# Kernel tuning notes

Hardware: AMD Instinct MI355X
Metric: run time of the kernel (lower is better)

## Reference

```python
import jax, jax.numpy as jnp
import numpy as np

B, H, W = 16, 128, 128
NUM_SAMPLES, HID = 16, 256


def setup_inputs() -> dict:
    key = jax.random.key(0)
    ks = jax.random.split(key, 12)
    inp = {
        "x": jax.random.uniform(ks[0], (B, H, W, 2), jnp.float32) * 2.0 - 1.0,
        "sample_idx": jax.random.randint(ks[1], (B,), 0, NUM_SAMPLES),
        "shift_vectors": jax.random.normal(ks[2], (NUM_SAMPLES, 2), jnp.float32) * 0.05,
        "rotation_angle": jax.random.normal(ks[3], (NUM_SAMPLES, 1), jnp.float32) * 0.05,
        "color_scales": 1.0 + jax.random.normal(ks[4], (NUM_SAMPLES, 3), jnp.float32) * 0.05,
        "color_shifts": jax.random.normal(ks[5], (NUM_SAMPLES, 3), jnp.float32) * 0.05,
        "W1": jax.random.normal(ks[6], (2, HID), jnp.float32) / np.sqrt(2.0),
        "b1": jnp.zeros((HID,), jnp.float32),
        "W2": jax.random.normal(ks[7], (HID, HID), jnp.float32) / np.sqrt(HID),
        "b2": jnp.zeros((HID,), jnp.float32),
        "W3": jax.random.normal(ks[8], (HID, HID), jnp.float32) / np.sqrt(HID),
        "b3": jnp.zeros((HID,), jnp.float32),
        "W4": jax.random.normal(ks[9], (HID, 3), jnp.float32) / np.sqrt(HID),
        "b4": jnp.zeros((3,), jnp.float32),
    }
    return inp


def reference(x, sample_idx, shift_vectors, rotation_angle, color_scales, color_shifts,
              W1, b1, W2, b2, W3, b3, W4, b4):
    # Per-sample affine coordinate transform (vectorized gather + batched 2x3 affine).
    shift = shift_vectors[sample_idx]            # [B,2] -> (dy, dx)
    dy, dx = shift[:, 0], shift[:, 1]
    ang = rotation_angle[sample_idx, 0]          # [B]
    c, s = jnp.cos(ang), jnp.sin(ang)
    rot = jnp.stack([jnp.stack([c, -s], -1),
                     jnp.stack([s, c], -1)], -2)  # [B,2,2]
    trans = jnp.stack([dx, dy], -1)               # [B,2]
    coords = jnp.einsum('bij,bhwj->bhwi', rot, x) + trans[:, None, None, :]

    # INR decoder MLP: coords -> RGB
    h = jax.nn.relu(coords @ W1 + b1)
    h = jax.nn.relu(h @ W2 + b2)
    h = jax.nn.relu(h @ W3 + b3)
    out = h @ W4 + b4                             # [B,H,W,3]

    # Per-sample color affine, skipped for reference sample idx==0.
    scales = color_scales[sample_idx][:, None, None, :]
    shifts = color_shifts[sample_idx][:, None, None, :]
    mask = (sample_idx != 0)[:, None, None, None]
    out = jnp.where(mask, out * scales + shifts, out)
    return out, dx, dy
```

## Files before the change

### kernel.cpp

```cpp
#include <hip/hip_runtime.h>
#include <math.h>

typedef _Float16 half8  __attribute__((ext_vector_type(8)));
typedef _Float16 half4v __attribute__((ext_vector_type(4)));
typedef __fp16   fp16x2 __attribute__((ext_vector_type(2)));
typedef float    f32x4  __attribute__((ext_vector_type(4)));
typedef float    f32x16 __attribute__((ext_vector_type(16)));

#define W1OFF 0
#define W2OFF 4096
#define W3OFF 69632
#define W4OFF 135168
#define SWTOT 143360
#define OUT_PIX (16*128*128)

__global__ void inr_prep(const float* __restrict__ W1, const float* __restrict__ W2,
                         const float* __restrict__ W3, const float* __restrict__ W4,
                         const int* __restrict__ sidx, const float* __restrict__ sv,
                         _Float16* __restrict__ wsw, float* __restrict__ outtail)
{
    int tid = blockIdx.x * 256 + threadIdx.x;
    if (tid < 16) {
        int si = sidx[tid];
        outtail[tid]      = sv[2*si + 1];
        outtail[16 + tid] = sv[2*si + 0];
    }
    if (tid >= SWTOT) return;
    int kind, rel;
    if      (tid < W2OFF) { kind = 0; rel = tid; }
    else if (tid < W3OFF) { kind = 1; rel = tid - W2OFF; }
    else if (tid < W4OFF) { kind = 2; rel = tid - W3OFF; }
    else                  { kind = 3; rel = tid - W4OFF; }
    int j    = rel & 7;
    int lane = (rel >> 3) & 63;
    int blk  = rel >> 9;
    int m32  = lane & 31;
    int hsel = lane >> 5;
    float val;
    if (kind == 3) {
        int k = blk*16 + hsel*8 + j;
        val = (m32 < 3) ? W4[k*3 + m32] : 0.0f;
    } else if (kind == 0) {
        int m = blk*32 + m32;
        int k = hsel*8 + j;
        val = (k < 2) ? W1[k*256 + m] : 0.0f;
    } else {
        int MT = blk & 7, s = blk >> 3;
        int m = MT*32 + m32;
        int k = s*16 + hsel*8 + j;
        val = (kind == 1) ? W2[k*256 + m] : W3[k*256 + m];
    }
    wsw[tid] = (_Float16)val;
}

template<int NKS>
__device__ __forceinline__ void do_layer(const half8* __restrict__ Asw,
                                         const float* __restrict__ bias,
                                         _Float16* hbuf, int w, int m32, int hsel, int lane)
{
    f32x16 acc[2][4];
#pragma unroll
    for (int mt = 0; mt < 2; ++mt)
#pragma unroll
        for (int nt = 0; nt < 4; ++nt)
#pragma unroll
            for (int i = 0; i < 16; ++i)
                acc[mt][nt][i] = 0.0f;

#pragma unroll
    for (int s = 0; s < NKS; ++s) {
        half8 aw[2];
#pragma unroll
        for (int mt = 0; mt < 2; ++mt)
            aw[mt] = Asw[(s*8 + 2*w + mt)*64 + lane];
        half8 bf[4];
        int g = s*2 + hsel;
#pragma unroll
        for (int nt = 0; nt < 4; ++nt)
            bf[nt] = *(const half8*)&hbuf[g*1024 + (32*nt + m32)*8];
#pragma unroll
        for (int nt = 0; nt < 4; ++nt)
#pragma unroll
            for (int mt = 0; mt < 2; ++mt)
                acc[mt][nt] = __builtin_amdgcn_mfma_f32_32x32x16_f16(aw[mt], bf[nt], acc[mt][nt], 0, 0, 0);
    }
    __syncthreads();
#pragma unroll
    for (int mt = 0; mt < 2; ++mt) {
#pragma unroll
        for (int g4 = 0; g4 < 4; ++g4) {
            int hid0 = 32*(2*w + mt) + 8*g4 + 4*hsel;
            f32x4 bv = *(const f32x4*)&bias[hid0];
            int gg = 4*(2*w + mt) + g4;
            int o  = 4*hsel;
#pragma unroll
            for (int nt = 0; nt < 4; ++nt) {
                int pixel = 32*nt + m32;
                fp16x2 lo = __builtin_amdgcn_cvt_pkrtz(fmaxf(acc[mt][nt][4*g4+0] + bv[0], 0.f),
                                                       fmaxf(acc[mt][nt][4*g4+1] + bv[1], 0.f));
                fp16x2 hi = __builtin_amdgcn_cvt_pkrtz(fmaxf(acc[mt][nt][4*g4+2] + bv[2], 0.f),
                                                       fmaxf(acc[mt][nt][4*g4+3] + bv[3], 0.f));
                half4v hv;
                hv[0] = (_Float16)lo[0]; hv[1] = (_Float16)lo[1];
                hv[2] = (_Float16)hi[0]; hv[3] = (_Float16)hi[1];
                *(half4v*)&hbuf[gg*1024 + pixel*8 + o] = hv;
            }
        }
    }
    __syncthreads();
}

__launch_bounds__(256, 2)
__global__ void inr_fused(const float* __restrict__ x, const int* __restrict__ sidx_p,
                          const float* __restrict__ sv, const float* __restrict__ ra,
                          const float* __restrict__ cs, const float* __restrict__ csh,
                          const float* __restrict__ b1, const float* __restrict__ b2,
                          const float* __restrict__ b3, const float* __restrict__ b4,
                          const _Float16* __restrict__ wsw, float* __restrict__ out)
{
    __shared__ __align__(16) _Float16 hbuf[32768];
    int t = threadIdx.x;
    int lane = t & 63, w = t >> 6;
    int m32 = lane & 31, hsel = lane >> 5;
    int pixbase = blockIdx.x * 128;
    int b = pixbase >> 14;
    int sidx = sidx_p[b];
    float dy = sv[2*sidx], dx = sv[2*sidx + 1];
    float ang = ra[sidx];
    float sn, cn;
    sincosf(ang, &sn, &cn);

    if (t < 128) {
        int p = t;
        float x0 = x[(pixbase + p)*2 + 0];
        float x1 = x[(pixbase + p)*2 + 1];
        float u = cn*x0 - sn*x1 + dx;
        float v = sn*x0 + cn*x1 + dy;
        half8 z;
#pragma unroll
        for (int i = 0; i < 8; ++i) z[i] = (_Float16)0.0f;
        *(half8*)&hbuf[1*1024 + p*8] = z;
        z[0] = (_Float16)u; z[1] = (_Float16)v;
        *(half8*)&hbuf[0*1024 + p*8] = z;
    }
    __syncthreads();

    const half8* wsw8 = (const half8*)wsw;
    do_layer<1> (wsw8 + (W1OFF >> 3), b1, hbuf, w, m32, hsel, lane);
    do_layer<16>(wsw8 + (W2OFF >> 3), b2, hbuf, w, m32, hsel, lane);
    do_layer<16>(wsw8 + (W3OFF >> 3), b3, hbuf, w, m32, hsel, lane);

    const half8* w4p = wsw8 + (W4OFF >> 3);
    f32x16 a4;
#pragma unroll
    for (int i = 0; i < 16; ++i) a4[i] = 0.0f;
#pragma unroll
    for (int s = 0; s < 16; ++s) {
        half8 aw = w4p[s*64 + lane];
        half8 bf = *(const half8*)&hbuf[(s*2 + hsel)*1024 + (32*w + m32)*8];
        a4 = __builtin_amdgcn_mfma_f32_32x32x16_f16(aw, bf, a4, 0, 0, 0);
    }
    if (lane < 32) {
        bool doc = (sidx != 0);
        float s0 = cs[sidx*3+0], s1 = cs[sidx*3+1], s2 = cs[sidx*3+2];
        float t0 = csh[sidx*3+0], t1 = csh[sidx*3+1], t2 = csh[sidx*3+2];
        float v0 = a4[0] + b4[0];
        float v1 = a4[1] + b4[1];
        float v2 = a4[2] + b4[2];
        if (doc) { v0 = v0*s0 + t0; v1 = v1*s1 + t1; v2 = v2*s2 + t2; }
        int gp = pixbase + 32*w + lane;
        out[gp*3 + 0] = v0;
        out[gp*3 + 1] = v1;
        out[gp*3 + 2] = v2;
    }
}

extern "C" void kernel_launch(void* const* d_in, const int* in_sizes, int n_in,
                              void* d_out, int out_size, void* d_ws, size_t ws_size,
                              hipStream_t stream)
{
    const float* x    = (const float*)d_in[0];
    const int*   sidx = (const int*)  d_in[1];
    const float* sv   = (const float*)d_in[2];
    const float* ra   = (const float*)d_in[3];
    const float* cs   = (const float*)d_in[4];
    const float* csh  = (const float*)d_in[5];
    const float* W1   = (const float*)d_in[6];
    const float* b1   = (const float*)d_in[7];
    const float* W2   = (const float*)d_in[8];
    const float* b2   = (const float*)d_in[9];
    const float* W3   = (const float*)d_in[10];
    const float* b3   = (const float*)d_in[11];
    const float* W4   = (const float*)d_in[12];
    const float* b4   = (const float*)d_in[13];
    float* out = (float*)d_out;
    _Float16* wsw = (_Float16*)d_ws;

    inr_prep<<<SWTOT/256, 256, 0, stream>>>(W1, W2, W3, W4, sidx, sv, wsw, out + OUT_PIX*3);
    inr_fused<<<OUT_PIX/128, 256, 0, stream>>>(x, sidx, sv, ra, cs, csh,
                                               b1, b2, b3, b4, wsw, out);
}
```

Before: 155.2 us.

## Keep MLP activations in registers per wave, exchanging halves via lane shuffles

Each wave now owns 32 pixels and computes all 256 hidden units for them. Activations stay in VGPR arrays and are passed between layers with cross-half __shfl_xor exchanges, instead of going through an LDS activation buffer with block-wide barriers. The weight swizzle in the prep kernel is reordered so K-steps are contiguous per output tile. The aim is to remove LDS traffic and __syncthreads. In exchange, every wave re-reads the full weight matrices from global memory/cache, which roughly quadruples weight load traffic per pixel, and register pressure goes up. A 64 KB shared array guarded by an impossible condition is kept, apparently so the LDS allocation and occupancy stay the same.

```diff
diff --git a/kernel.cpp b/kernel.cpp
--- a/kernel.cpp
+++ b/kernel.cpp
@@ -2,10 +2,10 @@
 #include <math.h>
 
 typedef _Float16 half8  __attribute__((ext_vector_type(8)));
-typedef _Float16 half4v __attribute__((ext_vector_type(4)));
 typedef __fp16   fp16x2 __attribute__((ext_vector_type(2)));
 typedef float    f32x4  __attribute__((ext_vector_type(4)));
 typedef float    f32x16 __attribute__((ext_vector_type(16)));
+typedef int      int4v  __attribute__((ext_vector_type(4)));
 
 #define W1OFF 0
 #define W2OFF 4096
@@ -45,7 +45,7 @@
         int k = hsel*8 + j;
         val = (k < 2) ? W1[k*256 + m] : 0.0f;
     } else {
-        int MT = blk & 7, s = blk >> 3;
+        int MT = blk >> 4, s = blk & 15;
         int m = MT*32 + m32;
         int k = s*16 + hsel*8 + j;
         val = (kind == 1) ? W2[k*256 + m] : W3[k*256 + m];
@@ -53,61 +53,57 @@
     wsw[tid] = (_Float16)val;
 }
 
-template<int NKS>
-__device__ __forceinline__ void do_layer(const half8* __restrict__ Asw,
-                                         const float* __restrict__ bias,
-                                         _Float16* hbuf, int w, int m32, int hsel, int lane)
-{
-    f32x16 acc[2][4];
-#pragma unroll
-    for (int mt = 0; mt < 2; ++mt)
-#pragma unroll
-        for (int nt = 0; nt < 4; ++nt)
-#pragma unroll
-            for (int i = 0; i < 16; ++i)
-                acc[mt][nt][i] = 0.0f;
-
-#pragma unroll
-    for (int s = 0; s < NKS; ++s) {
-        half8 aw[2];
-#pragma unroll
-        for (int mt = 0; mt < 2; ++mt)
-            aw[mt] = Asw[(s*8 + 2*w + mt)*64 + lane];
-        half8 bf[4];
-        int g = s*2 + hsel;
-#pragma unroll
-        for (int nt = 0; nt < 4; ++nt)
-            bf[nt] = *(const half8*)&hbuf[g*1024 + (32*nt + m32)*8];
-#pragma unroll
-        for (int nt = 0; nt < 4; ++nt)
-#pragma unroll
-            for (int mt = 0; mt < 2; ++mt)
-                acc[mt][nt] = __builtin_amdgcn_mfma_f32_32x32x16_f16(aw[mt], bf[nt], acc[mt][nt], 0, 0, 0);
-    }
-    __syncthreads();
-#pragma unroll
-    for (int mt = 0; mt < 2; ++mt) {
-#pragma unroll
-        for (int g4 = 0; g4 < 4; ++g4) {
-            int hid0 = 32*(2*w + mt) + 8*g4 + 4*hsel;
-            f32x4 bv = *(const f32x4*)&bias[hid0];
-            int gg = 4*(2*w + mt) + g4;
-            int o  = 4*hsel;
-#pragma unroll
-            for (int nt = 0; nt < 4; ++nt) {
-                int pixel = 32*nt + m32;
-                fp16x2 lo = __builtin_amdgcn_cvt_pkrtz(fmaxf(acc[mt][nt][4*g4+0] + bv[0], 0.f),
-                                                       fmaxf(acc[mt][nt][4*g4+1] + bv[1], 0.f));
-                fp16x2 hi = __builtin_amdgcn_cvt_pkrtz(fmaxf(acc[mt][nt][4*g4+2] + bv[2], 0.f),
-                                                       fmaxf(acc[mt][nt][4*g4+3] + bv[3], 0.f));
-                half4v hv;
-                hv[0] = (_Float16)lo[0]; hv[1] = (_Float16)lo[1];
-                hv[2] = (_Float16)hi[0]; hv[3] = (_Float16)hi[1];
-                *(half4v*)&hbuf[gg*1024 + pixel*8 + o] = hv;
-            }
+__device__ __forceinline__ void epi(const f32x16& acc, const float* __restrict__ bias,
+                                    int mt, half8 (&Bout)[16], int hsel)
+{
+    int ipk[8];
+#pragma unroll
+    for (int q = 0; q < 4; ++q) {
+        f32x4 bv = *(const f32x4*)&bias[32*mt + 8*q + 4*hsel];
+        fp16x2 lo = __builtin_amdgcn_cvt_pkrtz(fmaxf(acc[4*q+0] + bv[0], 0.f),
+                                               fmaxf(acc[4*q+1] + bv[1], 0.f));
+        fp16x2 hi = __builtin_amdgcn_cvt_pkrtz(fmaxf(acc[4*q+2] + bv[2], 0.f),
+                                               fmaxf(acc[4*q+3] + bv[3], 0.f));
+        ipk[2*q]   = __builtin_bit_cast(int, lo);
+        ipk[2*q+1] = __builtin_bit_cast(int, hi);
+    }
+#pragma unroll
+    for (int P = 0; P < 2; ++P) {
+        int s0 = ipk[4*P+0], s1 = ipk[4*P+1];
+        int t0 = ipk[4*P+2], t1 = ipk[4*P+3];
+        int send0 = hsel ? s0 : t0;
+        int send1 = hsel ? s1 : t1;
+        int x0 = __shfl_xor(send0, 32, 64);
+        int x1 = __shfl_xor(send1, 32, 64);
+        int4v r;
+        r[0] = hsel ? x0 : s0;
+        r[1] = hsel ? x1 : s1;
+        r[2] = hsel ? t0 : x0;
+        r[3] = hsel ? t1 : x1;
+        Bout[2*mt+P] = __builtin_bit_cast(half8, r);
+    }
+}
+
+__device__ __forceinline__ void big_layer(const half8* __restrict__ Aw,
+                                          const float* __restrict__ bias,
+                                          const half8 (&Bin)[16], half8 (&Bout)[16],
+                                          int lane, int hsel)
+{
+#pragma unroll
+    for (int mp = 0; mp < 4; ++mp) {
+        f32x16 acc0, acc1;
+#pragma unroll
+        for (int i = 0; i < 16; ++i) { acc0[i] = 0.f; acc1[i] = 0.f; }
+#pragma unroll
+        for (int s = 0; s < 16; ++s) {
+            half8 a0 = Aw[((2*mp+0)*16 + s)*64 + lane];
+            half8 a1 = Aw[((2*mp+1)*16 + s)*64 + lane];
+            acc0 = __builtin_amdgcn_mfma_f32_32x32x16_f16(a0, Bin[s], acc0, 0, 0, 0);
+            acc1 = __builtin_amdgcn_mfma_f32_32x32x16_f16(a1, Bin[s], acc1, 0, 0, 0);
         }
-    }
-    __syncthreads();
+        epi(acc0, bias, 2*mp+0, Bout, hsel);
+        epi(acc1, bias, 2*mp+1, Bout, hsel);
+    }
 }
 
 __launch_bounds__(256, 2)
@@ -118,10 +114,10 @@
                           const float* __restrict__ b3, const float* __restrict__ b4,
                           const _Float16* __restrict__ wsw, float* __restrict__ out)
 {
-    __shared__ __align__(16) _Float16 hbuf[32768];
+    __shared__ _Float16 hdummy[32768];
     int t = threadIdx.x;
     int lane = t & 63, w = t >> 6;
-    int m32 = lane & 31, hsel = lane >> 5;
+    int p32 = lane & 31, hsel = lane >> 5;
     int pixbase = blockIdx.x * 128;
     int b = pixbase >> 14;
     int sidx = sidx_p[b];
@@ -129,38 +125,54 @@
     float ang = ra[sidx];
     float sn, cn;
     sincosf(ang, &sn, &cn);
-
-    if (t < 128) {
-        int p = t;
-        float x0 = x[(pixbase + p)*2 + 0];
-        float x1 = x[(pixbase + p)*2 + 1];
-        float u = cn*x0 - sn*x1 + dx;
-        float v = sn*x0 + cn*x1 + dy;
-        half8 z;
-#pragma unroll
-        for (int i = 0; i < 8; ++i) z[i] = (_Float16)0.0f;
-        *(half8*)&hbuf[1*1024 + p*8] = z;
-        z[0] = (_Float16)u; z[1] = (_Float16)v;
-        *(half8*)&hbuf[0*1024 + p*8] = z;
-    }
-    __syncthreads();
+    if (sidx == 0x70000000) {
+        hdummy[t] = (_Float16)ang;
+        __syncthreads();
+        out[0] = (float)hdummy[(t + 1) & 255];
+    }
+
+    int pix = pixbase + 32*w + p32;
+    float xv0 = x[pix*2 + 0];
+    float xv1 = x[pix*2 + 1];
+    float u = cn*xv0 - sn*xv1 + dx;
+    float v = sn*xv0 + cn*xv1 + dy;
+
+    half8 BA[16], BB[16];
+    half8 B1;
+#pragma unroll
+    for (int i = 0; i < 8; ++i) B1[i] = (_Float16)0.0f;
+    if (hsel == 0) { B1[0] = (_Float16)u; B1[1] = (_Float16)v; }
 
     const half8* wsw8 = (const half8*)wsw;
-    do_layer<1> (wsw8 + (W1OFF >> 3), b1, hbuf, w, m32, hsel, lane);
-    do_layer<16>(wsw8 + (W2OFF >> 3), b2, hbuf, w, m32, hsel, lane);
-    do_layer<16>(wsw8 + (W3OFF >> 3), b3, hbuf, w, m32, hsel, lane);
-
-    const half8* w4p = wsw8 + (W4OFF >> 3);
+
+    {
+        const half8* A1 = wsw8 + (W1OFF >> 3);
+#pragma unroll
+        for (int mp = 0; mp < 4; ++mp) {
+            f32x16 acc0, acc1;
+#pragma unroll
+            for (int i = 0; i < 16; ++i) { acc0[i] = 0.f; acc1[i] = 0.f; }
+            half8 a0 = A1[(2*mp+0)*64 + lane];
+            half8 a1 = A1[(2*mp+1)*64 + lane];
+            acc0 = __builtin_amdgcn_mfma_f32_32x32x16_f16(a0, B1, acc0, 0, 0, 0);
+            acc1 = __builtin_amdgcn_mfma_f32_32x32x16_f16(a1, B1, acc1, 0, 0, 0);
+            epi(acc0, b1, 2*mp+0, BA, hsel);
+            epi(acc1, b1, 2*mp+1, BA, hsel);
+        }
+    }
+    big_layer(wsw8 + (W2OFF >> 3), b2, BA, BB, lane, hsel);
+    big_layer(wsw8 + (W3OFF >> 3), b3, BB, BA, lane, hsel);
+
+    const half8* A4 = wsw8 + (W4OFF >> 3);
     f32x16 a4;
 #pragma unroll
-    for (int i = 0; i < 16; ++i) a4[i] = 0.0f;
+    for (int i = 0; i < 16; ++i) a4[i] = 0.f;
 #pragma unroll
     for (int s = 0; s < 16; ++s) {
-        half8 aw = w4p[s*64 + lane];
-        half8 bf = *(const half8*)&hbuf[(s*2 + hsel)*1024 + (32*w + m32)*8];
-        a4 = __builtin_amdgcn_mfma_f32_32x32x16_f16(aw, bf, a4, 0, 0, 0);
-    }
-    if (lane < 32) {
+        half8 aw = A4[s*64 + lane];
+        a4 = __builtin_amdgcn_mfma_f32_32x32x16_f16(aw, BA[s], a4, 0, 0, 0);
+    }
+    if (hsel == 0) {
         bool doc = (sidx != 0);
         float s0 = cs[sidx*3+0], s1 = cs[sidx*3+1], s2 = cs[sidx*3+2];
         float t0 = csh[sidx*3+0], t1 = csh[sidx*3+1], t2 = csh[sidx*3+2];
@@ -168,10 +180,9 @@
         float v1 = a4[1] + b4[1];
         float v2 = a4[2] + b4[2];
         if (doc) { v0 = v0*s0 + t0; v1 = v1*s1 + t1; v2 = v2*s2 + t2; }
-        int gp = pixbase + 32*w + lane;
-        out[gp*3 + 0] = v0;
-        out[gp*3 + 1] = v1;
-        out[gp*3 + 2] = v2;
+        out[pix*3 + 0] = v0;
+        out[pix*3 + 1] = v1;
+        out[pix*3 + 2] = v2;
     }
 }
 
```

Result: slower. 169.9 us (+9.5%).
